# Kernel tuning notes

Measured on AMD Instinct MI355X. Metric: run time of the kernel, lower is better.

## Reference

```python
import jax, jax.numpy as jnp
import numpy as np

H, W = 480, 640
FLOW_SCALING = float(max(H, W))  # config default: max(resolution)
REGUL_WEIGHT = 0.001
MAX_TS = 1.0  # single association pass
EPS = 1e-9


def setup_inputs() -> dict:
    key = jax.random.key(0)
    k1, k2, k3, k4, k5 = jax.random.split(key, 5)
    B, N = 8, 131072
    # scale flow so warped displacements (flow * flow_scaling) are O(tens of px)
    flow = jax.random.normal(k1, (B, 2, H, W), jnp.float32) * 0.05
    ts = jax.random.uniform(k2, (B, N, 1), dtype=jnp.float32)
    ys = jax.random.randint(k3, (B, N), 0, H, dtype=jnp.int32)
    xs = jax.random.randint(k4, (B, N), 0, W, dtype=jnp.int32)
    pol = jax.random.randint(k5, (B, N), 0, 2, dtype=jnp.int32)  # 1 = positive event
    return {"flow": flow, "ts": ts, "ys": ys, "xs": xs, "pol": pol}


def _get_interpolation(ys, xs, ts0, fy, fx, tref):
    """Warp events to tref and build bilinear splat indices/weights.
    ys/xs: [B,N] int; ts0: [B,N] float; fy/fx: per-event flow [B,N].
    Returns idx [B,4N] int32 (flattened y*W+x) and weights [B,4N]."""
    dt = tref - ts0
    wy = ys.astype(jnp.float32) + dt * fy * FLOW_SCALING  # warped y [B,N]
    wx = xs.astype(jnp.float32) + dt * fx * FLOW_SCALING  # warped x [B,N]
    ty = jnp.floor(wy)
    by = ty + 1.0
    lx = jnp.floor(wx)
    rx = lx + 1.0
    # corner order: top-left, top-right, bottom-left, bottom-right -> [B,4N]
    iy = jnp.concatenate([ty, ty, by, by], axis=1)
    ix = jnp.concatenate([lx, rx, lx, rx], axis=1)
    wy4 = jnp.tile(wy, (1, 4))
    wx4 = jnp.tile(wx, (1, 4))
    w = jnp.maximum(0.0, 1.0 - jnp.abs(wy4 - iy)) * jnp.maximum(0.0, 1.0 - jnp.abs(wx4 - ix))
    inb = (iy >= 0) & (iy < H) & (ix >= 0) & (ix < W)
    iy = jnp.where(inb, iy, 0.0)
    ix = jnp.where(inb, ix, 0.0)
    w = w * inb.astype(w.dtype)
    idx = (iy * W + ix).astype(jnp.int32)
    return idx, w


def _splat(idx, w):
    """Scatter-add weights into per-pixel image. idx,w: [B,4N] -> [B,H*W]."""
    B = idx.shape[0]
    out = jnp.zeros((B, H * W), dtype=w.dtype)
    return out.at[jnp.arange(B)[:, None], idx].add(w)


def reference(flow, ts, ys, xs, pol):
    B, N = ys.shape
    # gather per-event flow (x channel 0, y channel 1) at original event pixels
    flat = ys * W + xs  # [B,N]
    flow_flat = flow.reshape(B, 2, H * W)
    bidx = jnp.arange(B)[:, None]
    fx = flow_flat[bidx, 0, flat]
    fy = flow_flat[bidx, 1, flat]

    ts0 = ts[..., 0]
    ts4 = jnp.tile(ts0, (1, 4))
    pos4 = jnp.tile(pol.astype(jnp.float32), (1, 4))
    neg4 = 1.0 - pos4

    def iwe_loss(tref, ts_w):
        idx, w = _get_interpolation(ys, xs, ts0, fy, fx, tref)
        iwe_pos = _splat(idx, w * pos4)
        iwe_neg = _splat(idx, w * neg4)
        iwe_pos_ts = _splat(idx, w * ts_w * pos4) / (iwe_pos + EPS) / MAX_TS
        iwe_neg_ts = _splat(idx, w * ts_w * neg4) / (iwe_neg + EPS) / MAX_TS
        l = jnp.sum(iwe_pos_ts ** 2, axis=1) + jnp.sum(iwe_neg_ts ** 2, axis=1)
        nz = jnp.sum(((iwe_pos + iwe_neg) > 0).astype(l.dtype), axis=1)
        return jnp.sum(l / nz)

    fw_loss = iwe_loss(MAX_TS, ts4)
    bw_loss = iwe_loss(0.0, MAX_TS - ts4)

    # flow smoothness (charbonnier over 4 spatial directions)
    fxm = flow[:, 0:1]
    fym = flow[:, 1:2]
    charb = lambda a, b: jnp.sqrt(a * a + b * b + 1e-6)
    dx = charb(fxm[..., :, :-1] - fxm[..., :, 1:], fym[..., :, :-1] - fym[..., :, 1:])
    dy = charb(fxm[..., :-1, :] - fxm[..., 1:, :], fym[..., :-1, :] - fym[..., 1:, :])
    dr = charb(fxm[..., :-1, :-1] - fxm[..., 1:, 1:], fym[..., :-1, :-1] - fym[..., 1:, 1:])
    ur = charb(fxm[..., 1:, :-1] - fxm[..., :-1, 1:], fym[..., 1:, :-1] - fym[..., :-1, 1:])
    smooth = (jnp.mean(dx) + jnp.mean(dy) + jnp.mean(dr) + jnp.mean(ur)) / 4.0

    return fw_loss + bw_loss + REGUL_WEIGHT * smooth
```

## Files before the change

kernel.cpp:

```cpp
#include <hip/hip_runtime.h>


constexpr int H = 480, W = 640, HW = H * W;
constexpr int B = 8, N = 131072;
constexpr float FLOW_SCALING = 640.0f;
constexpr float EPS = 1e-9f;

constexpr int TH = 48, TW = 64;
constexpr int TILES_Y = H / TH;
constexpr int TILES_X = W / TW;
constexpr int TILES = TILES_Y * TILES_X;
constexpr int NBINS = B * 2 * TILES;
constexpr int CAP = 4096;

constexpr float PSCALE = 262144.0f;
constexpr float PINV = 1.0f / 262144.0f;

constexpr int BND_BLK = 44;
constexpr int SM_BLK = 512;

constexpr int BPX = TILES_Y * W + TILES_X * H;

constexpr size_t ACCL_OFF = 0;
constexpr size_t ACCN_OFF = ACCL_OFF + (size_t)16 * TILES * 8;
constexpr size_t BNDL_OFF = ACCN_OFF + (size_t)16 * TILES * 8;
constexpr size_t BNDN_OFF = BNDL_OFF + (size_t)16 * BND_BLK * 8;
constexpr size_t SMP_OFF  = BNDN_OFF + (size_t)16 * BND_BLK * 8;
constexpr size_t CUR_OFF  = SMP_OFF + (size_t)SM_BLK * 4 * 8;
constexpr size_t BND_OFF  = CUR_OFF + (size_t)NBINS * 4;
constexpr size_t BND_BYTES = (size_t)16 * BPX * 2 * 8;
constexpr size_t ITEMS_OFF = BND_OFF + BND_BYTES;

__device__ inline double blk_reduce(double v, double* sm) {
    __syncthreads();
    #pragma unroll
    for (int o = 32; o > 0; o >>= 1) v += __shfl_down(v, o, 64);
    int lane = threadIdx.x & 63;
    int wid  = threadIdx.x >> 6;
    if (lane == 0) sm[wid] = v;
    __syncthreads();
    double r = 0.0;
    if (threadIdx.x == 0) {
        int nw = (int)(blockDim.x >> 6);
        for (int w2 = 0; w2 < nw; ++w2) r += sm[w2];
    }
    return r;
}

__device__ inline int bin_from_payload(unsigned long long v) {
    int t = (int)(v & 1);
    int fyi = (int)((unsigned)(v >> 40) >> 12) - 512;
    int fxi = (int)(((unsigned)(v >> 16) & 0xFFFFFFu) >> 12) - 512;
    int cy = min(max(fyi, 0), H - 1);
    int cx = min(max(fxi, 0), W - 1);
    return t * TILES + (cy / TH) * TILES_X + (cx >> 6);
}

__global__ __launch_bounds__(256) void scatter_kernel(
    const float* __restrict__ flow, const float* __restrict__ ts,
    const int* __restrict__ ys, const int* __restrict__ xs,
    const int* __restrict__ pol,
    unsigned long long* __restrict__ items, unsigned* __restrict__ cursors) {
    __shared__ unsigned long long sitems[4096];
    __shared__ unsigned scount[200];
    __shared__ unsigned sbase[200];
    __shared__ unsigned scur[200];
    int tid = threadIdx.x;
    for (int i = tid; i < 200; i += 256) { scount[i] = 0; scur[i] = 0; }
    __syncthreads();

    int b = blockIdx.x >> 6;
    int e0 = b * N + (blockIdx.x & 63) * 2048;
    const float* fb = flow + (size_t)b * 2 * HW;

    for (int k = 0; k < 8; ++k) {
        int ei = k * 256 + tid;
        int e = e0 + ei;
        int y = ys[e], x = xs[e], p = pol[e];
        float t0 = ts[e];
        int flat = y * W + x;
        float fx = fb[flat];
        float fy = fb[HW + flat];
        #pragma unroll
        for (int t = 0; t < 2; ++t) {
            float dt = (t == 0 ? 1.0f : 0.0f) - t0;
            float sw = (t == 0) ? t0 : 1.0f - t0;
            float wy = (float)y + dt * fy * FLOW_SCALING;
            float wx = (float)x + dt * fx * FLOW_SCALING;
            unsigned long long v = ~0ull;
            if (wy >= -1.0f && wy < (float)H && wx >= -1.0f && wx < (float)W) {
                unsigned uy = __float2uint_rn((wy + 512.0f) * 4096.0f);
                unsigned ux = __float2uint_rn((wx + 512.0f) * 4096.0f);
                unsigned usw = __float2uint_rn(sw * 16383.0f);
                v = ((unsigned long long)uy << 40) |
                    ((unsigned long long)ux << 16) |
                    ((unsigned long long)usw << 2) |
                    ((unsigned long long)(p != 0) << 1) |
                    (unsigned long long)t;
                atomicAdd(&scount[bin_from_payload(v)], 1u);
            }
            sitems[ei * 2 + t] = v;
        }
    }
    __syncthreads();
    if (tid < 200) {
        unsigned c = scount[tid];
        sbase[tid] = c ? atomicAdd(&cursors[b * 200 + tid], c) : 0u;
    }
    __syncthreads();
    for (int s = tid; s < 4096; s += 256) {
        unsigned long long v = sitems[s];
        if (v == ~0ull) continue;
        int binl = bin_from_payload(v);
        unsigned idx = sbase[binl] + atomicAdd(&scur[binl], 1u);
        if (idx < (unsigned)CAP)
            items[(size_t)(b * 200 + binl) * CAP + idx] = v;
    }
}

__global__ __launch_bounds__(256) void accum_kernel(
    const unsigned long long* __restrict__ items,
    const unsigned* __restrict__ cursors,
    unsigned long long* __restrict__ bnd,
    double* __restrict__ accL, double* __restrict__ accN) {
    constexpr int TPX = (TH + 1) * (TW + 1);
    __shared__ unsigned sacc[4 * TPX];
    __shared__ double sm[8];
    int tid = threadIdx.x;
    for (int i = tid; i < 4 * TPX; i += 256) sacc[i] = 0;
    __syncthreads();

    int bin = blockIdx.x;
    int b = bin / 200;
    int loc = bin - b * 200;
    int t = loc / TILES;
    int tile = loc - t * TILES;
    int y0 = (tile / TILES_X) * TH;
    int x0 = (tile % TILES_X) * TW;
    int cnt = (int)min(cursors[bin], (unsigned)CAP);
    const unsigned long long* bi = items + (size_t)bin * CAP;

    for (int i = tid; i < cnt; i += 256) {
        unsigned long long v = bi[i];
        unsigned uy = (unsigned)(v >> 40);
        unsigned ux = (unsigned)(v >> 16) & 0xFFFFFFu;
        float wy = (float)uy * (1.0f / 4096.0f) - 512.0f;
        float wx = (float)ux * (1.0f / 4096.0f) - 512.0f;
        int fyi = (int)(uy >> 12) - 512;
        int fxi = (int)(ux >> 12) - 512;
        float sw = (float)((unsigned)(v >> 2) & 0x3FFFu) * (1.0f / 16383.0f);
        int f = ((v >> 1) & 1) ? 0 : 2;
        #pragma unroll
        for (int dy = 0; dy < 2; ++dy) {
            int ry = fyi + dy, ly = ry - y0;
            if (ry < 0 || ry >= H || ly < 0 || ly > TH) continue;
            float wfy = 1.0f - fabsf(wy - (float)ry);
            #pragma unroll
            for (int dx = 0; dx < 2; ++dx) {
                int rx = fxi + dx, lx = rx - x0;
                if (rx < 0 || rx >= W || lx < 0 || lx > TW) continue;
                float wgt = wfy * (1.0f - fabsf(wx - (float)rx));
                int px = ly * (TW + 1) + lx;
                atomicAdd(&sacc[f * TPX + px], __float2uint_rn(wgt * PSCALE));
                atomicAdd(&sacc[(f + 1) * TPX + px],
                          __float2uint_rn(wgt * sw * PSCALE));
            }
        }
    }
    __syncthreads();

    double l = 0.0, nz = 0.0;
    unsigned long long* bj = bnd + (size_t)(b * 2 + t) * BPX * 2;
    for (int p = tid; p < TPX; p += 256) {
        int ly = p / (TW + 1), lx = p - ly * (TW + 1);
        int y = y0 + ly, x = x0 + lx;
        if (y >= H || x >= W) continue;
        unsigned wp = sacc[0 * TPX + p], sp = sacc[1 * TPX + p];
        unsigned wn = sacc[2 * TPX + p], sn = sacc[3 * TPX + p];
        if (ly == 0 || ly == TH) {
            int off = (y / TH) * W + x;
            if (wp | sp)
                atomicAdd(&bj[(size_t)off * 2],
                          ((unsigned long long)wp << 32) | sp);
            if (wn | sn)
                atomicAdd(&bj[(size_t)off * 2 + 1],
                          ((unsigned long long)wn << 32) | sn);
        } else if (lx == 0 || lx == TW) {
            int off = TILES_Y * W + (x >> 6) * H + y;
            if (wp | sp)
                atomicAdd(&bj[(size_t)off * 2],
                          ((unsigned long long)wp << 32) | sp);
            if (wn | sn)
                atomicAdd(&bj[(size_t)off * 2 + 1],
                          ((unsigned long long)wn << 32) | sn);
        } else {
            float fwp = (float)wp * PINV, fsp = (float)sp * PINV;
            float fwn = (float)wn * PINV, fsn = (float)sn * PINV;
            float a = fsp / (fwp + EPS);
            float c = fsn / (fwn + EPS);
            l += (double)(a * a + c * c);
            if (wp | wn) nz += 1.0;
        }
    }
    double lt = blk_reduce(l, sm);
    double nt = blk_reduce(nz, sm);
    if (tid == 0) {
        int j = b * 2 + t;
        accL[j * TILES + tile] = lt;
        accN[j * TILES + tile] = nt;
    }
}

__global__ __launch_bounds__(256) void bound_kernel(
    const unsigned long long* __restrict__ bnd,
    double* __restrict__ bndL, double* __restrict__ bndN) {
    __shared__ double sm[8];
    int j = blockIdx.y;
    double l = 0.0, nz = 0.0;
    for (int p = blockIdx.x * blockDim.x + threadIdx.x; p < BPX;
         p += gridDim.x * blockDim.x) {
        unsigned long long vp = bnd[((size_t)j * BPX + p) * 2];
        unsigned long long vn = bnd[((size_t)j * BPX + p) * 2 + 1];
        unsigned wp = (unsigned)(vp >> 32), sp = (unsigned)vp;
        unsigned wn = (unsigned)(vn >> 32), sn = (unsigned)vn;
        float a = ((float)sp * PINV) / ((float)wp * PINV + EPS);
        float c = ((float)sn * PINV) / ((float)wn * PINV + EPS);
        l += (double)(a * a + c * c);
        if (wp | wn) nz += 1.0;
    }
    double lt = blk_reduce(l, sm);
    double nt = blk_reduce(nz, sm);
    if (threadIdx.x == 0) {
        bndL[j * BND_BLK + blockIdx.x] = lt;
        bndN[j * BND_BLK + blockIdx.x] = nt;
    }
}

__device__ inline float charb(float a, float b) {
    return sqrtf(a * a + b * b + 1e-6f);
}

__global__ __launch_bounds__(256) void smooth_kernel(
    const float* __restrict__ flow, double* __restrict__ smP) {
    __shared__ double sm[8];
    double sdx = 0.0, sdy = 0.0, sdr = 0.0, sur = 0.0;
    int stride = gridDim.x * blockDim.x;
    for (int i = blockIdx.x * blockDim.x + threadIdx.x; i < B * HW; i += stride) {
        int b = i / HW;
        int rem = i - b * HW;
        int y = rem / W;
        int x = rem - y * W;
        const float* fx = flow + (size_t)(b * 2 + 0) * HW;
        const float* fy = flow + (size_t)(b * 2 + 1) * HW;
        float f00 = fx[rem], g00 = fy[rem];
        bool xe = (x + 1) < W;
        bool ye = (y + 1) < H;
        if (xe) {
            float f01 = fx[rem + 1], g01 = fy[rem + 1];
            sdx += (double)charb(f00 - f01, g00 - g01);
            if (ye) {
                float f10 = fx[rem + W], g10 = fy[rem + W];
                float f11 = fx[rem + W + 1], g11 = fy[rem + W + 1];
                sdy += (double)charb(f00 - f10, g00 - g10);
                sdr += (double)charb(f00 - f11, g00 - g11);
                sur += (double)charb(f10 - f01, g10 - g01);
            }
        } else if (ye) {
            float f10 = fx[rem + W], g10 = fy[rem + W];
            sdy += (double)charb(f00 - f10, g00 - g10);
        }
    }
    double tt;
    tt = blk_reduce(sdx, sm); if (threadIdx.x == 0) smP[blockIdx.x * 4 + 0] = tt;
    tt = blk_reduce(sdy, sm); if (threadIdx.x == 0) smP[blockIdx.x * 4 + 1] = tt;
    tt = blk_reduce(sdr, sm); if (threadIdx.x == 0) smP[blockIdx.x * 4 + 2] = tt;
    tt = blk_reduce(sur, sm); if (threadIdx.x == 0) smP[blockIdx.x * 4 + 3] = tt;
}

__global__ __launch_bounds__(256) void final_kernel(
    const double* __restrict__ accL, const double* __restrict__ accN,
    const double* __restrict__ bndL, const double* __restrict__ bndN,
    const double* __restrict__ smP, float* __restrict__ out) {
    __shared__ double sj[16];
    __shared__ double sm[8];
    int tid = threadIdx.x;
    int j = tid >> 4, s = tid & 15;
    double l = 0.0, nz = 0.0;
    for (int i = s; i < TILES; i += 16) {
        l += accL[j * TILES + i];
        nz += accN[j * TILES + i];
    }
    for (int i = s; i < BND_BLK; i += 16) {
        l += bndL[j * BND_BLK + i];
        nz += bndN[j * BND_BLK + i];
    }
    #pragma unroll
    for (int o = 8; o > 0; o >>= 1) {
        l += __shfl_down(l, o, 16);
        nz += __shfl_down(nz, o, 16);
    }
    if (s == 0) sj[j] = l / nz;

    double c[4] = {0.0, 0.0, 0.0, 0.0};
    for (int i = tid; i < SM_BLK; i += 256) {
        #pragma unroll
        for (int k = 0; k < 4; ++k) c[k] += smP[i * 4 + k];
    }
    double s0 = blk_reduce(c[0], sm);
    double s1 = blk_reduce(c[1], sm);
    double s2 = blk_reduce(c[2], sm);
    double s3 = blk_reduce(c[3], sm);
    __syncthreads();
    if (tid == 0) {
        double loss = 0.0;
        for (int q = 0; q < 16; ++q) loss += sj[q];
        double ndx = (double)B * H * (W - 1);
        double ndy = (double)B * (H - 1) * W;
        double ndd = (double)B * (H - 1) * (W - 1);
        double smooth = (s0 / ndx + s1 / ndy + s2 / ndd + s3 / ndd) * 0.25;
        out[0] = (float)(loss + 0.001 * smooth);
    }
}

extern "C" void kernel_launch(void* const* d_in, const int* in_sizes, int n_in,
                              void* d_out, int out_size, void* d_ws, size_t ws_size,
                              hipStream_t stream) {
    const float* flow = (const float*)d_in[0];
    const float* ts   = (const float*)d_in[1];
    const int*   ys   = (const int*)d_in[2];
    const int*   xs   = (const int*)d_in[3];
    const int*   pol  = (const int*)d_in[4];
    float* out = (float*)d_out;

    char* ws = (char*)d_ws;
    double* accL = (double*)(ws + ACCL_OFF);
    double* accN = (double*)(ws + ACCN_OFF);
    double* bndL = (double*)(ws + BNDL_OFF);
    double* bndN = (double*)(ws + BNDN_OFF);
    double* smP  = (double*)(ws + SMP_OFF);
    unsigned* cursors = (unsigned*)(ws + CUR_OFF);
    unsigned long long* bnd = (unsigned long long*)(ws + BND_OFF);
    unsigned long long* items = (unsigned long long*)(ws + ITEMS_OFF);

    hipMemsetAsync(ws + CUR_OFF, 0, ITEMS_OFF - CUR_OFF, stream);
    smooth_kernel<<<SM_BLK, 256, 0, stream>>>(flow, smP);
    scatter_kernel<<<512, 256, 0, stream>>>(flow, ts, ys, xs, pol, items, cursors);
    accum_kernel<<<NBINS, 256, 0, stream>>>(items, cursors, bnd, accL, accN);
    bound_kernel<<<dim3(BND_BLK, 16), 256, 0, stream>>>(bnd, bndL, bndN);
    final_kernel<<<1, 256, 0, stream>>>(accL, accN, bndL, bndN, smP, out);
}
```

Measured before the change: 178.6 us.

## Keep scatter payloads in registers and pack LDS splat accumulators into 64-bit

The scatter kernel now handles 1024 events per block across 1024 blocks, interleaved by batch, and keeps its eight payloads in registers instead of a 32 KB shared staging array. This frees LDS so more blocks can be resident. The accumulation kernel packs the weight and timestamp-weight sums into one 64-bit shared word per pixel and polarity, so each corner costs one 64-bit LDS atomic instead of two 32-bit ones. The packing relies on the low 32-bit sum never overflowing into the high half, and doubling the block count also doubles the number of global cursor atomics.

```diff
diff --git a/kernel.cpp b/kernel.cpp
--- a/kernel.cpp
+++ b/kernel.cpp
@@ -18,6 +18,7 @@
 
 constexpr int BND_BLK = 44;
 constexpr int SM_BLK = 512;
+constexpr int SC_BLOCKS = 1024;
 
 constexpr int BPX = TILES_Y * W + TILES_X * H;
 
@@ -61,21 +62,22 @@
     const int* __restrict__ ys, const int* __restrict__ xs,
     const int* __restrict__ pol,
     unsigned long long* __restrict__ items, unsigned* __restrict__ cursors) {
-    __shared__ unsigned long long sitems[4096];
     __shared__ unsigned scount[200];
     __shared__ unsigned sbase[200];
     __shared__ unsigned scur[200];
     int tid = threadIdx.x;
-    for (int i = tid; i < 200; i += 256) { scount[i] = 0; scur[i] = 0; }
-    __syncthreads();
-
-    int b = blockIdx.x >> 6;
-    int e0 = b * N + (blockIdx.x & 63) * 2048;
+    if (tid < 200) { scount[tid] = 0; scur[tid] = 0; }
+    __syncthreads();
+
+    int b = blockIdx.x & 7;
+    int chunk = blockIdx.x >> 3;
+    int e0 = b * N + chunk * 1024;
     const float* fb = flow + (size_t)b * 2 * HW;
 
-    for (int k = 0; k < 8; ++k) {
-        int ei = k * 256 + tid;
-        int e = e0 + ei;
+    unsigned long long pay[8];
+    #pragma unroll
+    for (int k = 0; k < 4; ++k) {
+        int e = e0 + k * 256 + tid;
         int y = ys[e], x = xs[e], p = pol[e];
         float t0 = ts[e];
         int flat = y * W + x;
@@ -99,7 +101,7 @@
                     (unsigned long long)t;
                 atomicAdd(&scount[bin_from_payload(v)], 1u);
             }
-            sitems[ei * 2 + t] = v;
+            pay[k * 2 + t] = v;
         }
     }
     __syncthreads();
@@ -108,8 +110,9 @@
         sbase[tid] = c ? atomicAdd(&cursors[b * 200 + tid], c) : 0u;
     }
     __syncthreads();
-    for (int s = tid; s < 4096; s += 256) {
-        unsigned long long v = sitems[s];
+    #pragma unroll
+    for (int i = 0; i < 8; ++i) {
+        unsigned long long v = pay[i];
         if (v == ~0ull) continue;
         int binl = bin_from_payload(v);
         unsigned idx = sbase[binl] + atomicAdd(&scur[binl], 1u);
@@ -124,10 +127,10 @@
     unsigned long long* __restrict__ bnd,
     double* __restrict__ accL, double* __restrict__ accN) {
     constexpr int TPX = (TH + 1) * (TW + 1);
-    __shared__ unsigned sacc[4 * TPX];
+    __shared__ unsigned long long sacc[2 * TPX];
     __shared__ double sm[8];
     int tid = threadIdx.x;
-    for (int i = tid; i < 4 * TPX; i += 256) sacc[i] = 0;
+    for (int i = tid; i < 2 * TPX; i += 256) sacc[i] = 0ull;
     __syncthreads();
 
     int bin = blockIdx.x;
@@ -149,7 +152,7 @@
         int fyi = (int)(uy >> 12) - 512;
         int fxi = (int)(ux >> 12) - 512;
         float sw = (float)((unsigned)(v >> 2) & 0x3FFFu) * (1.0f / 16383.0f);
-        int f = ((v >> 1) & 1) ? 0 : 2;
+        int f = ((v >> 1) & 1) ? 0 : 1;
         #pragma unroll
         for (int dy = 0; dy < 2; ++dy) {
             int ry = fyi + dy, ly = ry - y0;
@@ -161,9 +164,10 @@
                 if (rx < 0 || rx >= W || lx < 0 || lx > TW) continue;
                 float wgt = wfy * (1.0f - fabsf(wx - (float)rx));
                 int px = ly * (TW + 1) + lx;
-                atomicAdd(&sacc[f * TPX + px], __float2uint_rn(wgt * PSCALE));
-                atomicAdd(&sacc[(f + 1) * TPX + px],
-                          __float2uint_rn(wgt * sw * PSCALE));
+                unsigned w18 = __float2uint_rn(wgt * PSCALE);
+                unsigned s18 = __float2uint_rn(wgt * sw * PSCALE);
+                atomicAdd(&sacc[f * TPX + px],
+                          ((unsigned long long)w18 << 32) | s18);
             }
         }
     }
@@ -175,31 +179,25 @@
         int ly = p / (TW + 1), lx = p - ly * (TW + 1);
         int y = y0 + ly, x = x0 + lx;
         if (y >= H || x >= W) continue;
-        unsigned wp = sacc[0 * TPX + p], sp = sacc[1 * TPX + p];
-        unsigned wn = sacc[2 * TPX + p], sn = sacc[3 * TPX + p];
+        unsigned long long vp = sacc[p];
+        unsigned long long vn = sacc[TPX + p];
         if (ly == 0 || ly == TH) {
             int off = (y / TH) * W + x;
-            if (wp | sp)
-                atomicAdd(&bj[(size_t)off * 2],
-                          ((unsigned long long)wp << 32) | sp);
-            if (wn | sn)
-                atomicAdd(&bj[(size_t)off * 2 + 1],
-                          ((unsigned long long)wn << 32) | sn);
+            if (vp) atomicAdd(&bj[(size_t)off * 2], vp);
+            if (vn) atomicAdd(&bj[(size_t)off * 2 + 1], vn);
         } else if (lx == 0 || lx == TW) {
             int off = TILES_Y * W + (x >> 6) * H + y;
-            if (wp | sp)
-                atomicAdd(&bj[(size_t)off * 2],
-                          ((unsigned long long)wp << 32) | sp);
-            if (wn | sn)
-                atomicAdd(&bj[(size_t)off * 2 + 1],
-                          ((unsigned long long)wn << 32) | sn);
+            if (vp) atomicAdd(&bj[(size_t)off * 2], vp);
+            if (vn) atomicAdd(&bj[(size_t)off * 2 + 1], vn);
         } else {
-            float fwp = (float)wp * PINV, fsp = (float)sp * PINV;
-            float fwn = (float)wn * PINV, fsn = (float)sn * PINV;
+            float fwp = (float)(unsigned)(vp >> 32) * PINV;
+            float fsp = (float)(unsigned)vp * PINV;
+            float fwn = (float)(unsigned)(vn >> 32) * PINV;
+            float fsn = (float)(unsigned)vn * PINV;
             float a = fsp / (fwp + EPS);
             float c = fsn / (fwn + EPS);
             l += (double)(a * a + c * c);
-            if (wp | wn) nz += 1.0;
+            if ((vp | vn) >> 32) nz += 1.0;
         }
     }
     double lt = blk_reduce(l, sm);
@@ -344,7 +342,7 @@
 
     hipMemsetAsync(ws + CUR_OFF, 0, ITEMS_OFF - CUR_OFF, stream);
     smooth_kernel<<<SM_BLK, 256, 0, stream>>>(flow, smP);
-    scatter_kernel<<<512, 256, 0, stream>>>(flow, ts, ys, xs, pol, items, cursors);
+    scatter_kernel<<<SC_BLOCKS, 256, 0, stream>>>(flow, ts, ys, xs, pol, items, cursors);
     accum_kernel<<<NBINS, 256, 0, stream>>>(items, cursors, bnd, accL, accN);
     bound_kernel<<<dim3(BND_BLK, 16), 256, 0, stream>>>(bnd, bndL, bndN);
     final_kernel<<<1, 256, 0, stream>>>(accL, accN, bndL, bndN, smP, out);
```

New measurement: 159.0 us. 11.0% less time.
